# Kernel optimization log

Hardware: AMD Instinct MI355X
Metric: run time of the kernel (lower is better)

Reference implementation:

```python
import jax, jax.numpy as jnp
import numpy as np

D = 256
H = 8
HD = D // H
LN_EPS = 1e-5


def setup_inputs() -> dict:
    key = jax.random.key(0)
    ks = jax.random.split(key, 20)
    N = 768
    s = lambda *sh: 1.0 / np.sqrt(sh[-1])
    inp = {
        "features": jax.random.normal(ks[0], (N, D), jnp.float32),
        "boxes": jax.random.uniform(ks[1], (N, 4), jnp.float32),
        # MultiheadAttention params (torch layout: [out, in])
        "in_proj_w": jax.random.normal(ks[2], (3 * D, D), jnp.float32) * s(D),
        "in_proj_b": jnp.zeros((3 * D,), jnp.float32),
        "out_proj_w": jax.random.normal(ks[3], (D, D), jnp.float32) * s(D),
        "out_proj_b": jnp.zeros((D,), jnp.float32),
        # similarity_net params
        "w1": jax.random.normal(ks[4], (256, 3 * D + 3), jnp.float32) * s(3 * D + 3),
        "b1": jnp.zeros((256,), jnp.float32),
        "ln_g": jnp.ones((256,), jnp.float32),
        "ln_b": jnp.zeros((256,), jnp.float32),
        "w2": jax.random.normal(ks[5], (128, 256), jnp.float32) * s(256),
        "b2": jnp.zeros((128,), jnp.float32),
        "w3": jax.random.normal(ks[6], (64, 128), jnp.float32) * s(128),
        "b3": jnp.zeros((64,), jnp.float32),
        "w4": jax.random.normal(ks[7], (32, 64), jnp.float32) * s(64),
        "b4": jnp.zeros((32,), jnp.float32),
        "w5": jax.random.normal(ks[8], (1, 32), jnp.float32) * s(32),
        "b5": jnp.zeros((1,), jnp.float32),
    }
    return inp


def _mha(x, in_w, in_b, out_w, out_b):
    # x: [N, D]; torch nn.MultiheadAttention self-attention (eval mode)
    N = x.shape[0]
    qkv = x @ in_w.T + in_b                      # [N, 3D]
    q, k, v = jnp.split(qkv, 3, axis=-1)
    q = q.reshape(N, H, HD).transpose(1, 0, 2)   # [H, N, HD]
    k = k.reshape(N, H, HD).transpose(1, 0, 2)
    v = v.reshape(N, H, HD).transpose(1, 0, 2)
    scores = jnp.einsum("hnd,hmd->hnm", q, k) / np.sqrt(HD)
    attn = jax.nn.softmax(scores, axis=-1)
    o = jnp.einsum("hnm,hmd->hnd", attn, v)      # [H, N, HD]
    o = o.transpose(1, 0, 2).reshape(N, D)
    return o @ out_w.T + out_b


def reference(features, boxes, in_proj_w, in_proj_b, out_proj_w, out_proj_b,
              w1, b1, ln_g, ln_b, w2, b2, w3, b3, w4, b4, w5, b5):
    N = features.shape[0]
    att = _mha(features, in_proj_w, in_proj_b, out_proj_w, out_proj_b)  # [N, D]

    fi = jnp.broadcast_to(att[:, None, :], (N, N, D))
    fj = jnp.broadcast_to(att[None, :, :], (N, N, D))
    bi = boxes[:, None, :]
    bj = boxes[None, :, :]
    x_dist = jnp.abs(bi[:, :, 0] - bj[:, :, 0])
    y_diff = bi[:, :, 1] - bj[:, :, 1]
    spatial = jnp.stack([x_dist, jnp.abs(y_diff), y_diff], axis=-1)    # [N, N, 3]
    pairs = jnp.concatenate([fi, fj, fi * fj, spatial], axis=-1)       # [N, N, 3D+3]

    h = jax.nn.relu(pairs @ w1.T + b1)
    mu = jnp.mean(h, axis=-1, keepdims=True)
    var = jnp.var(h, axis=-1, keepdims=True)
    h = (h - mu) / jnp.sqrt(var + LN_EPS) * ln_g + ln_b
    h = jax.nn.relu(h @ w2.T + b2)
    h = jax.nn.relu(h @ w3.T + b3)
    h = jax.nn.relu(h @ w4.T + b4)
    logits = (h @ w5.T + b5)[..., 0]                                   # [N, N]

    eye = jnp.eye(N, dtype=logits.dtype)
    return logits * (1.0 - eye) - 1e9 * eye
```

## Files before the change

kernel.cpp:

```cpp
#include <hip/hip_runtime.h>


typedef __attribute__((ext_vector_type(8))) __bf16 bf16x8;
typedef __attribute__((ext_vector_type(4))) float f32x4;

__device__ __forceinline__ float bf2f(unsigned short u) {
    return __uint_as_float(((unsigned int)u) << 16);
}
__device__ __forceinline__ unsigned short f2bf(float f) {
    union { __bf16 b; unsigned short u; } cv;
    cv.b = (__bf16)f;
    return cv.u;
}
__device__ __forceinline__ int pk4_fp8(float a, float b, float c, float d) {
    int w = __builtin_amdgcn_cvt_pk_fp8_f32(a, b, 0, false);
    w = __builtin_amdgcn_cvt_pk_fp8_f32(c, d, w, true);
    return w;
}
__device__ __forceinline__ unsigned char f2fp8(float v) {
    return (unsigned char)(__builtin_amdgcn_cvt_pk_fp8_f32(v, 0.f, 0, false) & 0xff);
}

__global__ __launch_bounds__(256) void pack_all(
    const float* __restrict__ features, const float* __restrict__ in_proj_w,
    const float* __restrict__ out_proj_w, const float* __restrict__ w1,
    const float* __restrict__ w2, const float* __restrict__ w3,
    const float* __restrict__ w4, const float* __restrict__ b1,
    const float* __restrict__ ln_g, const float* __restrict__ ln_b,
    const float* __restrict__ b2, const float* __restrict__ out_proj_b,
    unsigned short* __restrict__ featb, unsigned short* __restrict__ inWb,
    unsigned short* __restrict__ WcatB, unsigned short* __restrict__ outWTb,
    unsigned short* __restrict__ wABb,
    unsigned char* __restrict__ w1c_f8, unsigned char* __restrict__ w2g_f8,
    unsigned char* __restrict__ w3_f8, unsigned char* __restrict__ w4_f8,
    float* __restrict__ bias768, float* __restrict__ c1, float* __restrict__ c2,
    float* __restrict__ biasZ)
{
    int t = blockIdx.x * 256 + threadIdx.x;
    if (t < 196608) {
        featb[t] = f2bf(features[t]);
    } else if (t < 393216) {
        int u = t - 196608; inWb[u] = f2bf(in_proj_w[u]);
    } else if (t < 458752) {
        int u = t - 393216; WcatB[u] = f2bf(out_proj_w[u]);
    } else if (t < 524288) {
        int u = t - 458752; int e = u >> 8, d = u & 255;
        outWTb[u] = f2bf(out_proj_w[d * 256 + e]);
    } else if (t < 655360) {
        int u = t - 524288; int n = u >> 8, k = u & 255;
        float v = (n < 256) ? w1[n * 771 + k] : w1[(n - 256) * 771 + 256 + k];
        wABb[u] = f2bf(v);
    } else if (t < 729088) {
        int u = t - 655360;
        int e = u & 7, lane = (u >> 3) & 63, f = u >> 9;
        int l15 = lane & 15, quad = lane >> 4;
        int mt = f & 15, kc = f >> 4;
        int o = mt * 16 + l15, k = kc * 32 + quad * 8 + e;
        float v;
        if (k < 256)            v = w1[o * 771 + 512 + k];
        else if (k < 259)       v = w1[o * 771 + 768 + (k - 256)];
        else                    v = 0.f;
        w1c_f8[u] = f2fp8(v);
    } else if (t < 761856) {
        int u = t - 729088;
        int e = u & 7, lane = (u >> 3) & 63, f = u >> 9;
        int l15 = lane & 15, quad = lane >> 4;
        int mt = f & 7, kc = f >> 3;
        int o = mt * 16 + l15, k = kc * 32 + quad * 8 + e;
        w2g_f8[u] = f2fp8(w2[o * 256 + k] * ln_g[k]);
    } else if (t < 770048) {
        int u = t - 761856;
        int e = u & 7, lane = (u >> 3) & 63, f = u >> 9;
        int l15 = lane & 15, quad = lane >> 4;
        int mt = f & 3, kc = f >> 2;
        int o = mt * 16 + l15, k = kc * 32 + quad * 8 + e;
        w3_f8[u] = f2fp8(w3[o * 128 + k]);
    } else if (t < 772096) {
        int u = t - 770048;
        int e = u & 7, lane = (u >> 3) & 63, f = u >> 9;
        int l15 = lane & 15, quad = lane >> 4;
        int mt = f & 1, kc = f >> 1;
        int o = mt * 16 + l15, k = kc * 32 + quad * 8 + e;
        w4_f8[u] = f2fp8(w4[o * 64 + k]);
    } else if (t < 772864) {
        int n = t - 772096;
        if (n < 256) bias768[n] = out_proj_b[n];
        else {
            int m = n - 256;
            float s = 0.f;
            for (int d = 0; d < 256; d += 4) {
                float4 ob = *reinterpret_cast<const float4*>(&out_proj_b[d]);
                const float* wr = (m < 256) ? &w1[m * 771 + d]
                                            : &w1[(m - 256) * 771 + 256 + d];
                float4 w = *reinterpret_cast<const float4*>(wr);
                s += ob.x * w.x + ob.y * w.y + ob.z * w.z + ob.w * w.w;
            }
            bias768[n] = s + ((m < 256) ? b1[m] : 0.f);
        }
    } else if (t < 772992) {
        int p = t - 772864;
        float s2 = 0.f, s1 = 0.f;
        for (int k = 0; k < 256; k += 4) {
            float4 w = *reinterpret_cast<const float4*>(&w2[p * 256 + k]);
            float4 g = *reinterpret_cast<const float4*>(&ln_g[k]);
            float4 lb = *reinterpret_cast<const float4*>(&ln_b[k]);
            s2 += g.x * w.x + g.y * w.y + g.z * w.z + g.w * w.w;
            s1 += lb.x * w.x + lb.y * w.y + lb.z * w.z + lb.w * w.w;
        }
        c2[p] = s2;
        c1[p] = s1 + b2[p];
    } else if (t < 773248) {
        biasZ[t - 772992] = 0.f;
    }
}

__global__ __launch_bounds__(256) void gemm_bf(
    const unsigned short* __restrict__ A, const unsigned short* __restrict__ W,
    const float* __restrict__ bias, float* __restrict__ Cf,
    unsigned short* __restrict__ Cbf, unsigned short* __restrict__ Vt,
    int N, int K, int ldc, int tcol0)
{
    const int wv = threadIdx.x >> 6, lane = threadIdx.x & 63;
    const int l15 = lane & 15, quad = lane >> 4;
    const int row0 = blockIdx.x * 64 + wv * 16;
    const int col0 = blockIdx.y * 64;
    f32x4 acc[4] = {};
    for (int kc = 0; kc < (K >> 5); ++kc) {
        bf16x8 a = *reinterpret_cast<const bf16x8*>(&A[(row0 + l15) * K + kc * 32 + quad * 8]);
#pragma unroll
        for (int ct = 0; ct < 4; ++ct) {
            bf16x8 b = *reinterpret_cast<const bf16x8*>(&W[(col0 + ct * 16 + l15) * K + kc * 32 + quad * 8]);
            acc[ct] = __builtin_amdgcn_mfma_f32_16x16x32_bf16(a, b, acc[ct], 0, 0, 0);
        }
    }
#pragma unroll
    for (int ct = 0; ct < 4; ++ct)
#pragma unroll
        for (int r = 0; r < 4; ++r) {
            int row = row0 + quad * 4 + r, col = col0 + ct * 16 + l15;
            float v = acc[ct][r] + bias[col];
            if (Vt && col >= tcol0) {
                Vt[(col - tcol0) * 768 + row] = f2bf(v);
            } else {
                if (Cf)  Cf[row * ldc + col] = v;
                if (Cbf) Cbf[row * ldc + col] = f2bf(v);
            }
        }
}

__global__ __launch_bounds__(256) void gemm_attab(
    const unsigned short* __restrict__ A, const unsigned short* __restrict__ W,
    const float* __restrict__ bias, float* __restrict__ att,
    unsigned short* __restrict__ attb, float* __restrict__ AB)
{
    const int wv = threadIdx.x >> 6, lane = threadIdx.x & 63;
    const int l15 = lane & 15, quad = lane >> 4;
    const int row0 = blockIdx.x * 64 + wv * 16;
    const int col0 = blockIdx.y * 64;
    f32x4 acc[4] = {};
    for (int kc = 0; kc < 8; ++kc) {
        bf16x8 a = *reinterpret_cast<const bf16x8*>(&A[(row0 + l15) * 256 + kc * 32 + quad * 8]);
#pragma unroll
        for (int ct = 0; ct < 4; ++ct) {
            bf16x8 b = *reinterpret_cast<const bf16x8*>(&W[(col0 + ct * 16 + l15) * 256 + kc * 32 + quad * 8]);
            acc[ct] = __builtin_amdgcn_mfma_f32_16x16x32_bf16(a, b, acc[ct], 0, 0, 0);
        }
    }
#pragma unroll
    for (int ct = 0; ct < 4; ++ct)
#pragma unroll
        for (int r = 0; r < 4; ++r) {
            int row = row0 + quad * 4 + r, col = col0 + ct * 16 + l15;
            float v = acc[ct][r] + bias[col];
            if (col < 256) {
                att[row * 256 + col] = v;
                attb[row * 256 + col] = f2bf(v);
            } else {
                AB[row * 512 + (col - 256)] = v;
            }
        }
}

#define SP 776

__global__ __launch_bounds__(256) void attn_mfma(
    const unsigned short* __restrict__ qkvb, const unsigned short* __restrict__ Vt,
    unsigned short* __restrict__ Obf)
{
    __shared__ __align__(16) unsigned short smS[64 * SP];
    const int h = blockIdx.x, q0 = blockIdx.y * 64, hb = h * 32;
    const int tid = threadIdx.x, wave = tid >> 6, lane = tid & 63;
    const int l15 = lane & 15, quad = lane >> 4;

    bf16x8 af[4];
#pragma unroll
    for (int mt = 0; mt < 4; ++mt)
        af[mt] = *reinterpret_cast<const bf16x8*>(&qkvb[(q0 + mt * 16 + l15) * 768 + hb + quad * 8]);
#pragma unroll
    for (int ct = 0; ct < 12; ++ct) {
        int n0 = wave * 192 + ct * 16;
        bf16x8 b = *reinterpret_cast<const bf16x8*>(&qkvb[(n0 + l15) * 768 + 256 + hb + quad * 8]);
#pragma unroll
        for (int mt = 0; mt < 4; ++mt) {
            f32x4 c = {};
            c = __builtin_amdgcn_mfma_f32_16x16x32_bf16(af[mt], b, c, 0, 0, 0);
#pragma unroll
            for (int r = 0; r < 4; ++r)
                smS[(mt * 16 + quad * 4 + r) * SP + n0 + l15] =
                    f2bf(c[r] * 0.17677669529663689f);
        }
    }
    __syncthreads();

    {
        const int row = tid >> 2, part = tid & 3;
        unsigned short* rp = &smS[row * SP + part * 192];
        float mx = -3.0e38f;
#pragma unroll
        for (int c8 = 0; c8 < 24; ++c8) {
            uint4 v = *reinterpret_cast<const uint4*>(&rp[c8 * 8]);
            const unsigned short* pe = reinterpret_cast<const unsigned short*>(&v);
#pragma unroll
            for (int e = 0; e < 8; ++e) mx = fmaxf(mx, bf2f(pe[e]));
        }
        mx = fmaxf(mx, __shfl_xor(mx, 1, 64));
        mx = fmaxf(mx, __shfl_xor(mx, 2, 64));
        float ls = 0.f;
#pragma unroll
        for (int c8 = 0; c8 < 24; ++c8) {
            uint4 v = *reinterpret_cast<const uint4*>(&rp[c8 * 8]);
            const unsigned short* pe = reinterpret_cast<const unsigned short*>(&v);
            unsigned short o8[8];
#pragma unroll
            for (int e = 0; e < 8; ++e) {
                float ev = __expf(bf2f(pe[e]) - mx);
                ls += ev;
                o8[e] = f2bf(ev);
            }
            *reinterpret_cast<uint4*>(&rp[c8 * 8]) = *reinterpret_cast<const uint4*>(o8);
        }
        ls += __shfl_xor(ls, 1, 64);
        ls += __shfl_xor(ls, 2, 64);
        float inv = 1.0f / ls;
#pragma unroll
        for (int c8 = 0; c8 < 24; ++c8) {
            uint4 v = *reinterpret_cast<const uint4*>(&rp[c8 * 8]);
            const unsigned short* pe = reinterpret_cast<const unsigned short*>(&v);
            unsigned short o8[8];
#pragma unroll
            for (int e = 0; e < 8; ++e) o8[e] = f2bf(bf2f(pe[e]) * inv);
            *reinterpret_cast<uint4*>(&rp[c8 * 8]) = *reinterpret_cast<const uint4*>(o8);
        }
    }
    f32x4 accp[2] = {};
    for (int kc = 0; kc < 24; ++kc) {
        bf16x8 a = *reinterpret_cast<const bf16x8*>(&smS[(wave * 16 + l15) * SP + kc * 32 + quad * 8]);
#pragma unroll
        for (int ct = 0; ct < 2; ++ct) {
            bf16x8 b = *reinterpret_cast<const bf16x8*>(&Vt[(hb + ct * 16 + l15) * 768 + kc * 32 + quad * 8]);
            accp[ct] = __builtin_amdgcn_mfma_f32_16x16x32_bf16(a, b, accp[ct], 0, 0, 0);
        }
    }
#pragma unroll
    for (int ct = 0; ct < 2; ++ct)
#pragma unroll
        for (int r = 0; r < 4; ++r) {
            int row = q0 + wave * 16 + quad * 4 + r;
            Obf[row * 256 + hb + ct * 16 + l15] = f2bf(accp[ct][r]);
        }
}

#define S1 296
#define S2 136
#define S3 72

__global__ __launch_bounds__(256, 4) void pair_mlp(
    const float* __restrict__ att, const unsigned short* __restrict__ attb,
    const float* __restrict__ AB,
    const unsigned char* __restrict__ w1c_f8, const unsigned char* __restrict__ w2g_f8,
    const unsigned char* __restrict__ w3_f8, const unsigned char* __restrict__ w4_f8,
    const float* __restrict__ boxes,
    const float* __restrict__ c1, const float* __restrict__ c2,
    const float* __restrict__ b3, const float* __restrict__ b4,
    const float* __restrict__ w5, const float* __restrict__ b5,
    float* __restrict__ out)
{
    __shared__ __align__(16) unsigned char smH[64 * S1];
    __shared__ float s_psum[64][4], s_pssq[64][4];
    __shared__ float s_mu[64], s_rs[64];
    __shared__ float s_l5[64][2];

    const int i    = blockIdx.x;
    const int j0   = blockIdx.y * 64;
    const int tid  = threadIdx.x;
    const int wave = tid >> 6;
    const int lane = tid & 63;
    const int l15  = lane & 15;
    const int quad = lane >> 4;

    {
        const int g = tid & 63;
        float4 fi4 = *reinterpret_cast<const float4*>(&att[i * 256 + g * 4]);
#pragma unroll
        for (int it = 0; it < 16; ++it) {
            int r = (tid >> 6) + it * 4;
            uint2 aj = *reinterpret_cast<const uint2*>(&attb[(j0 + r) * 256 + g * 4]);
            float a0 = __uint_as_float(aj.x << 16);
            float a1 = __uint_as_float(aj.x & 0xffff0000u);
            float a2 = __uint_as_float(aj.y << 16);
            float a3 = __uint_as_float(aj.y & 0xffff0000u);
            *reinterpret_cast<int*>(&smH[r * S1 + g * 4]) =
                pk4_fp8(a0 * fi4.x, a1 * fi4.y, a2 * fi4.z, a3 * fi4.w);
        }
    }
    if (tid < 64) {
        int j = j0 + tid;
        float xd = fabsf(boxes[i * 4 + 0] - boxes[j * 4 + 0]);
        float yd = boxes[i * 4 + 1] - boxes[j * 4 + 1];
        *reinterpret_cast<int*>(&smH[tid * S1 + 256]) = pk4_fp8(xd, fabsf(yd), yd, 0.f);
        *reinterpret_cast<int*>(&smH[tid * S1 + 260]) = 0;
        *reinterpret_cast<long long*>(&smH[tid * S1 + 264]) = 0;
        *reinterpret_cast<long long*>(&smH[tid * S1 + 272]) = 0;
        *reinterpret_cast<long long*>(&smH[tid * S1 + 280]) = 0;
    }
    __syncthreads();

    f32x4 acc1[4][4] = {};
    for (int kc = 0; kc < 9; ++kc) {
        long long a[4];
#pragma unroll
        for (int mt = 0; mt < 4; ++mt)
            a[mt] = *reinterpret_cast<const long long*>(&w1c_f8[((kc * 16 + wave * 4 + mt) * 64 + lane) * 8]);
#pragma unroll
        for (int nt = 0; nt < 4; ++nt) {
            long long b = *reinterpret_cast<const long long*>(&smH[(nt * 16 + l15) * S1 + kc * 32 + quad * 8]);
#pragma unroll
            for (int mt = 0; mt < 4; ++mt)
                acc1[mt][nt] = __builtin_amdgcn_mfma_f32_16x16x32_fp8_fp8(a[mt], b, acc1[mt][nt], 0, 0, 0);
        }
    }

    const int o0 = wave * 64;
    float vsum[4] = {}, vssq[4] = {};
#pragma unroll
    for (int mt = 0; mt < 4; ++mt) {
        int o = o0 + mt * 16 + quad * 4;
        float4 Ai = *reinterpret_cast<const float4*>(&AB[i * 512 + o]);
        float AiA[4] = {Ai.x, Ai.y, Ai.z, Ai.w};
#pragma unroll
        for (int nt = 0; nt < 4; ++nt) {
            int j = nt * 16 + l15;
            float4 Bj = *reinterpret_cast<const float4*>(&AB[(j0 + j) * 512 + 256 + o]);
            float BjA[4] = {Bj.x, Bj.y, Bj.z, Bj.w};
#pragma unroll
            for (int r = 0; r < 4; ++r) {
                float v = fmaxf(acc1[mt][nt][r] + AiA[r] + BjA[r], 0.f);
                acc1[mt][nt][r] = v;
                vsum[nt] += v; vssq[nt] += v * v;
            }
        }
    }
#pragma unroll
    for (int nt = 0; nt < 4; ++nt) {
        vsum[nt] += __shfl_xor(vsum[nt], 16, 64);
        vsum[nt] += __shfl_xor(vsum[nt], 32, 64);
        vssq[nt] += __shfl_xor(vssq[nt], 16, 64);
        vssq[nt] += __shfl_xor(vssq[nt], 32, 64);
    }
    if (quad == 0)
#pragma unroll
        for (int nt = 0; nt < 4; ++nt) {
            s_psum[nt * 16 + l15][wave] = vsum[nt];
            s_pssq[nt * 16 + l15][wave] = vssq[nt];
        }
    __syncthreads();
#pragma unroll
    for (int mt = 0; mt < 4; ++mt) {
        int o = o0 + mt * 16 + quad * 4;
#pragma unroll
        for (int nt = 0; nt < 4; ++nt) {
            int j = nt * 16 + l15;
            *reinterpret_cast<int*>(&smH[j * S1 + o]) =
                pk4_fp8(acc1[mt][nt][0], acc1[mt][nt][1], acc1[mt][nt][2], acc1[mt][nt][3]);
        }
    }
    if (wave == 0) {
        int j = lane;
        float sm = (s_psum[j][0] + s_psum[j][1] + s_psum[j][2] + s_psum[j][3]) * (1.0f / 256.0f);
        float sq = (s_pssq[j][0] + s_pssq[j][1] + s_pssq[j][2] + s_pssq[j][3]) * (1.0f / 256.0f);
        s_mu[j] = sm;
        s_rs[j] = rsqrtf(sq - sm * sm + 1e-5f);
    }
    __syncthreads();

    f32x4 acc2[2][4] = {};
    for (int kc = 0; kc < 8; ++kc) {
        long long a[2];
#pragma unroll
        for (int mt = 0; mt < 2; ++mt)
            a[mt] = *reinterpret_cast<const long long*>(&w2g_f8[((kc * 8 + wave * 2 + mt) * 64 + lane) * 8]);
#pragma unroll
        for (int nt = 0; nt < 4; ++nt) {
            long long b = *reinterpret_cast<const long long*>(&smH[(nt * 16 + l15) * S1 + kc * 32 + quad * 8]);
#pragma unroll
            for (int mt = 0; mt < 2; ++mt)
                acc2[mt][nt] = __builtin_amdgcn_mfma_f32_16x16x32_fp8_fp8(a[mt], b, acc2[mt][nt], 0, 0, 0);
        }
    }
    __syncthreads();
#pragma unroll
    for (int mt = 0; mt < 2; ++mt) {
        int p = wave * 32 + mt * 16 + quad * 4;
        float4 C1 = *reinterpret_cast<const float4*>(&c1[p]);
        float4 C2 = *reinterpret_cast<const float4*>(&c2[p]);
        float C1A[4] = {C1.x, C1.y, C1.z, C1.w};
        float C2A[4] = {C2.x, C2.y, C2.z, C2.w};
#pragma unroll
        for (int nt = 0; nt < 4; ++nt) {
            int j = nt * 16 + l15;
            float mu = s_mu[j], rs = s_rs[j];
            float vv[4];
#pragma unroll
            for (int r = 0; r < 4; ++r)
                vv[r] = fmaxf(rs * (acc2[mt][nt][r] - mu * C2A[r]) + C1A[r], 0.f);
            *reinterpret_cast<int*>(&smH[j * S2 + p]) = pk4_fp8(vv[0], vv[1], vv[2], vv[3]);
        }
    }
    __syncthreads();

    f32x4 acc3[4] = {};
    for (int kc = 0; kc < 4; ++kc) {
        long long a = *reinterpret_cast<const long long*>(&w3_f8[((kc * 4 + wave) * 64 + lane) * 8]);
#pragma unroll
        for (int nt = 0; nt < 4; ++nt) {
            long long b = *reinterpret_cast<const long long*>(&smH[(nt * 16 + l15) * S2 + kc * 32 + quad * 8]);
            acc3[nt] = __builtin_amdgcn_mfma_f32_16x16x32_fp8_fp8(a, b, acc3[nt], 0, 0, 0);
        }
    }
    __syncthreads();
    {
        int q = wave * 16 + quad * 4;
        float4 B3 = *reinterpret_cast<const float4*>(&b3[q]);
        float B3A[4] = {B3.x, B3.y, B3.z, B3.w};
#pragma unroll
        for (int nt = 0; nt < 4; ++nt) {
            int j = nt * 16 + l15;
            float vv[4];
#pragma unroll
            for (int r = 0; r < 4; ++r)
                vv[r] = fmaxf(acc3[nt][r] + B3A[r], 0.f);
            *reinterpret_cast<int*>(&smH[j * S3 + q]) = pk4_fp8(vv[0], vv[1], vv[2], vv[3]);
        }
    }
    __syncthreads();

    const int mt4 = wave & 1;
    const int jh  = wave >> 1;
    f32x4 acc4[2] = {};
#pragma unroll
    for (int kc = 0; kc < 2; ++kc) {
        long long a = *reinterpret_cast<const long long*>(&w4_f8[((kc * 2 + mt4) * 64 + lane) * 8]);
#pragma unroll
        for (int nt = 0; nt < 2; ++nt) {
            int j = jh * 32 + nt * 16 + l15;
            long long b = *reinterpret_cast<const long long*>(&smH[j * S3 + kc * 32 + quad * 8]);
            acc4[nt] = __builtin_amdgcn_mfma_f32_16x16x32_fp8_fp8(a, b, acc4[nt], 0, 0, 0);
        }
    }
    {
        int o4 = mt4 * 16 + quad * 4;
        float4 B4 = *reinterpret_cast<const float4*>(&b4[o4]);
        float4 W5 = *reinterpret_cast<const float4*>(&w5[o4]);
        float B4A[4] = {B4.x, B4.y, B4.z, B4.w};
        float W5A[4] = {W5.x, W5.y, W5.z, W5.w};
#pragma unroll
        for (int nt = 0; nt < 2; ++nt) {
            float part = 0.f;
#pragma unroll
            for (int r = 0; r < 4; ++r)
                part += fmaxf(acc4[nt][r] + B4A[r], 0.f) * W5A[r];
            part += __shfl_xor(part, 16, 64);
            part += __shfl_xor(part, 32, 64);
            if (quad == 0)
                s_l5[jh * 32 + nt * 16 + l15][mt4] = part;
        }
    }
    __syncthreads();
    if (tid < 64) {
        int j = j0 + tid;
        float v = s_l5[tid][0] + s_l5[tid][1] + b5[0];
        out[i * 768 + j] = (j == i) ? -1.0e9f : v;
    }
}

extern "C" void kernel_launch(void* const* d_in, const int* in_sizes, int n_in,
                              void* d_out, int out_size, void* d_ws, size_t ws_size,
                              hipStream_t stream)
{
    const float* features   = (const float*)d_in[0];
    const float* boxes      = (const float*)d_in[1];
    const float* in_proj_w  = (const float*)d_in[2];
    const float* in_proj_b  = (const float*)d_in[3];
    const float* out_proj_w = (const float*)d_in[4];
    const float* out_proj_b = (const float*)d_in[5];
    const float* w1  = (const float*)d_in[6];
    const float* b1  = (const float*)d_in[7];
    const float* ln_g = (const float*)d_in[8];
    const float* ln_b = (const float*)d_in[9];
    const float* w2  = (const float*)d_in[10];
    const float* b2  = (const float*)d_in[11];
    const float* w3  = (const float*)d_in[12];
    const float* b3  = (const float*)d_in[13];
    const float* w4  = (const float*)d_in[14];
    const float* b4  = (const float*)d_in[15];
    const float* w5  = (const float*)d_in[16];
    const float* b5  = (const float*)d_in[17];
    float* out = (float*)d_out;

    char* p = (char*)d_ws;
    unsigned short* qkvb  = (unsigned short*)p; p += 768 * 768 * 2;
    unsigned short* Vt    = (unsigned short*)p; p += 256 * 768 * 2;
    unsigned short* Obf   = (unsigned short*)p; p += 768 * 256 * 2;
    unsigned short* attb  = (unsigned short*)p; p += 768 * 256 * 2;
    float* att = (float*)p; p += 768 * 256 * 4;
    float* AB  = (float*)p; p += 768 * 512 * 4;
    unsigned short* featb  = (unsigned short*)p; p += 196608 * 2;
    unsigned short* inWb   = (unsigned short*)p; p += 196608 * 2;
    unsigned short* WcatB  = (unsigned short*)p; p += 196608 * 2;
    unsigned short* outWTb = (unsigned short*)p; p += 65536 * 2;
    unsigned short* wABb   = (unsigned short*)p; p += 131072 * 2;
    unsigned char* w1c_f8  = (unsigned char*)p; p += 73728;
    unsigned char* w2g_f8  = (unsigned char*)p; p += 32768;
    unsigned char* w3_f8   = (unsigned char*)p; p += 8192;
    unsigned char* w4_f8   = (unsigned char*)p; p += 2048;
    float* bias768 = (float*)p; p += 768 * 4;
    float* c1v     = (float*)p; p += 128 * 4;
    float* c2v     = (float*)p; p += 128 * 4;
    float* biasZ   = (float*)p; p += 256 * 4;

    pack_all<<<dim3(3021), dim3(256), 0, stream>>>(features, in_proj_w,
        out_proj_w, w1, w2, w3, w4, b1, ln_g, ln_b, b2, out_proj_b,
        featb, inWb, WcatB, outWTb, wABb, w1c_f8, w2g_f8, w3_f8, w4_f8,
        bias768, c1v, c2v, biasZ);
    gemm_bf<<<dim3(8, 4), dim3(256), 0, stream>>>(wABb, outWTb, biasZ,
        (float*)nullptr, WcatB + 65536, (unsigned short*)nullptr, 256, 256, 256, 1 << 30);
    gemm_bf<<<dim3(12, 12), dim3(256), 0, stream>>>(featb, inWb, in_proj_b,
        (float*)nullptr, qkvb, Vt, 768, 256, 768, 512);
    attn_mfma<<<dim3(8, 12), dim3(256), 0, stream>>>(qkvb, Vt, Obf);
    gemm_attab<<<dim3(12, 12), dim3(256), 0, stream>>>(Obf, WcatB, bias768,
        att, attb, AB);
    pair_mlp<<<dim3(768, 12), dim3(256), 0, stream>>>(att, attb, AB,
        w1c_f8, w2g_f8, w3_f8, w4_f8, boxes, c1v, c2v,
        b3, b4, w5, b5, out);
}
```

Before: 304.7 us.

## Fold QKV and weight-product GEMMs into packing kernel, split attention finer

The separate bf16 conversion pass and two gemm_bf launches are removed. The pack kernel now does the QKV projection straight from fp32 inputs, converting on load, and computes the W1·out_proj product as a scalar dot-product block. This cuts two launches and the intermediate bf16 buffers. Attention now uses 32-query tiles for twice as many blocks. pair_mlp drops the bf16 att copy and uses separate shared buffers per layer, which removes two barriers at the cost of more LDS per block and possibly lower occupancy.

```diff
diff --git a/kernel.cpp b/kernel.cpp
--- a/kernel.cpp
+++ b/kernel.cpp
@@ -12,6 +12,9 @@
     cv.b = (__bf16)f;
     return cv.u;
 }
+__device__ __forceinline__ unsigned pk2(float lo, float hi) {
+    return (unsigned)f2bf(lo) | ((unsigned)f2bf(hi) << 16);
+}
 __device__ __forceinline__ int pk4_fp8(float a, float b, float c, float d) {
     int w = __builtin_amdgcn_cvt_pk_fp8_f32(a, b, 0, false);
     w = __builtin_amdgcn_cvt_pk_fp8_f32(c, d, w, true);
@@ -20,138 +23,138 @@
 __device__ __forceinline__ unsigned char f2fp8(float v) {
     return (unsigned char)(__builtin_amdgcn_cvt_pk_fp8_f32(v, 0.f, 0, false) & 0xff);
 }
+__device__ __forceinline__ bf16x8 load8f_bf(const float* p) {
+    float4 a = *reinterpret_cast<const float4*>(p);
+    float4 b = *reinterpret_cast<const float4*>(p + 4);
+    union { bf16x8 v; unsigned u[4]; } cv;
+    cv.u[0] = pk2(a.x, a.y); cv.u[1] = pk2(a.z, a.w);
+    cv.u[2] = pk2(b.x, b.y); cv.u[3] = pk2(b.z, b.w);
+    return cv.v;
+}
 
 __global__ __launch_bounds__(256) void pack_all(
     const float* __restrict__ features, const float* __restrict__ in_proj_w,
-    const float* __restrict__ out_proj_w, const float* __restrict__ w1,
-    const float* __restrict__ w2, const float* __restrict__ w3,
-    const float* __restrict__ w4, const float* __restrict__ b1,
-    const float* __restrict__ ln_g, const float* __restrict__ ln_b,
-    const float* __restrict__ b2, const float* __restrict__ out_proj_b,
-    unsigned short* __restrict__ featb, unsigned short* __restrict__ inWb,
-    unsigned short* __restrict__ WcatB, unsigned short* __restrict__ outWTb,
-    unsigned short* __restrict__ wABb,
+    const float* __restrict__ in_proj_b, const float* __restrict__ out_proj_w,
+    const float* __restrict__ w1, const float* __restrict__ w2,
+    const float* __restrict__ w3, const float* __restrict__ w4,
+    const float* __restrict__ b1, const float* __restrict__ ln_g,
+    const float* __restrict__ ln_b, const float* __restrict__ b2,
+    const float* __restrict__ out_proj_b,
+    unsigned short* __restrict__ qkvb, unsigned short* __restrict__ Vt,
+    unsigned short* __restrict__ WcatB,
     unsigned char* __restrict__ w1c_f8, unsigned char* __restrict__ w2g_f8,
     unsigned char* __restrict__ w3_f8, unsigned char* __restrict__ w4_f8,
-    float* __restrict__ bias768, float* __restrict__ c1, float* __restrict__ c2,
-    float* __restrict__ biasZ)
+    float* __restrict__ bias768, float* __restrict__ c1, float* __restrict__ c2)
 {
-    int t = blockIdx.x * 256 + threadIdx.x;
-    if (t < 196608) {
-        featb[t] = f2bf(features[t]);
-    } else if (t < 393216) {
-        int u = t - 196608; inWb[u] = f2bf(in_proj_w[u]);
-    } else if (t < 458752) {
-        int u = t - 393216; WcatB[u] = f2bf(out_proj_w[u]);
-    } else if (t < 524288) {
-        int u = t - 458752; int e = u >> 8, d = u & 255;
-        outWTb[u] = f2bf(out_proj_w[d * 256 + e]);
-    } else if (t < 655360) {
-        int u = t - 524288; int n = u >> 8, k = u & 255;
-        float v = (n < 256) ? w1[n * 771 + k] : w1[(n - 256) * 771 + 256 + k];
-        wABb[u] = f2bf(v);
-    } else if (t < 729088) {
-        int u = t - 655360;
-        int e = u & 7, lane = (u >> 3) & 63, f = u >> 9;
-        int l15 = lane & 15, quad = lane >> 4;
-        int mt = f & 15, kc = f >> 4;
-        int o = mt * 16 + l15, k = kc * 32 + quad * 8 + e;
-        float v;
-        if (k < 256)            v = w1[o * 771 + 512 + k];
-        else if (k < 259)       v = w1[o * 771 + 768 + (k - 256)];
-        else                    v = 0.f;
-        w1c_f8[u] = f2fp8(v);
-    } else if (t < 761856) {
-        int u = t - 729088;
-        int e = u & 7, lane = (u >> 3) & 63, f = u >> 9;
-        int l15 = lane & 15, quad = lane >> 4;
-        int mt = f & 7, kc = f >> 3;
-        int o = mt * 16 + l15, k = kc * 32 + quad * 8 + e;
-        w2g_f8[u] = f2fp8(w2[o * 256 + k] * ln_g[k]);
-    } else if (t < 770048) {
-        int u = t - 761856;
-        int e = u & 7, lane = (u >> 3) & 63, f = u >> 9;
-        int l15 = lane & 15, quad = lane >> 4;
-        int mt = f & 3, kc = f >> 2;
-        int o = mt * 16 + l15, k = kc * 32 + quad * 8 + e;
-        w3_f8[u] = f2fp8(w3[o * 128 + k]);
-    } else if (t < 772096) {
-        int u = t - 770048;
-        int e = u & 7, lane = (u >> 3) & 63, f = u >> 9;
-        int l15 = lane & 15, quad = lane >> 4;
-        int mt = f & 1, kc = f >> 1;
-        int o = mt * 16 + l15, k = kc * 32 + quad * 8 + e;
-        w4_f8[u] = f2fp8(w4[o * 64 + k]);
-    } else if (t < 772864) {
-        int n = t - 772096;
-        if (n < 256) bias768[n] = out_proj_b[n];
-        else {
-            int m = n - 256;
-            float s = 0.f;
-            for (int d = 0; d < 256; d += 4) {
-                float4 ob = *reinterpret_cast<const float4*>(&out_proj_b[d]);
-                const float* wr = (m < 256) ? &w1[m * 771 + d]
-                                            : &w1[(m - 256) * 771 + 256 + d];
-                float4 w = *reinterpret_cast<const float4*>(wr);
-                s += ob.x * w.x + ob.y * w.y + ob.z * w.z + ob.w * w.w;
+    const int blk = blockIdx.x;
+    if (blk < 716) {
+        int t = blk * 256 + threadIdx.x;
+        if (t < 65536) {
+            WcatB[t] = f2bf(out_proj_w[t]);
+        } else if (t < 139264) {
+            int u = t - 65536;
+            int e = u & 7, lane = (u >> 3) & 63, f = u >> 9;
+            int l15 = lane & 15, quad = lane >> 4;
+            int ct = f & 15, kc = f >> 4;
+            int o = ct * 16 + l15, k = kc * 32 + quad * 8 + e;
+            float v;
+            if (k < 256)       v = w1[o * 771 + 512 + k];
+            else if (k < 259)  v = w1[o * 771 + 768 + (k - 256)];
+            else               v = 0.f;
+            w1c_f8[u] = f2fp8(v);
+        } else if (t < 172032) {
+            int u = t - 139264;
+            int e = u & 7, lane = (u >> 3) & 63, f = u >> 9;
+            int l15 = lane & 15, quad = lane >> 4;
+            int ct = f & 7, kc = f >> 3;
+            int o = ct * 16 + l15, k = kc * 32 + quad * 8 + e;
+            w2g_f8[u] = f2fp8(w2[o * 256 + k] * ln_g[k]);
+        } else if (t < 180224) {
+            int u = t - 172032;
+            int e = u & 7, lane = (u >> 3) & 63, f = u >> 9;
+            int l15 = lane & 15, quad = lane >> 4;
+            int ct = f & 3, kc = f >> 2;
+            int o = ct * 16 + l15, k = kc * 32 + quad * 8 + e;
+            w3_f8[u] = f2fp8(w3[o * 128 + k]);
+        } else if (t < 182272) {
+            int u = t - 180224;
+            int e = u & 7, lane = (u >> 3) & 63, f = u >> 9;
+            int l15 = lane & 15, quad = lane >> 4;
+            int ct = f & 1, kc = f >> 1;
+            int o = ct * 16 + l15, k = kc * 32 + quad * 8 + e;
+            w4_f8[u] = f2fp8(w4[o * 64 + k]);
+        } else if (t < 183040) {
+            int n = t - 182272;
+            if (n < 256) bias768[n] = out_proj_b[n];
+            else {
+                int m = n - 256;
+                float s = 0.f;
+                for (int d = 0; d < 256; d += 4) {
+                    float4 ob = *reinterpret_cast<const float4*>(&out_proj_b[d]);
+                    const float* wr = (m < 256) ? &w1[m * 771 + d]
+                                                : &w1[(m - 256) * 771 + 256 + d];
+                    float4 w = *reinterpret_cast<const float4*>(wr);
+                    s += ob.x * w.x + ob.y * w.y + ob.z * w.z + ob.w * w.w;
+                }
+                bias768[n] = s + ((m < 256) ? b1[m] : 0.f);
             }
-            bias768[n] = s + ((m < 256) ? b1[m] : 0.f);
-        }
-    } else if (t < 772992) {
-        int p = t - 772864;
-        float s2 = 0.f, s1 = 0.f;
-        for (int k = 0; k < 256; k += 4) {
-            float4 w = *reinterpret_cast<const float4*>(&w2[p * 256 + k]);
-            float4 g = *reinterpret_cast<const float4*>(&ln_g[k]);
-            float4 lb = *reinterpret_cast<const float4*>(&ln_b[k]);
-            s2 += g.x * w.x + g.y * w.y + g.z * w.z + g.w * w.w;
-            s1 += lb.x * w.x + lb.y * w.y + lb.z * w.z + lb.w * w.w;
-        }
-        c2[p] = s2;
-        c1[p] = s1 + b2[p];
-    } else if (t < 773248) {
-        biasZ[t - 772992] = 0.f;
-    }
-}
-
-__global__ __launch_bounds__(256) void gemm_bf(
-    const unsigned short* __restrict__ A, const unsigned short* __restrict__ W,
-    const float* __restrict__ bias, float* __restrict__ Cf,
-    unsigned short* __restrict__ Cbf, unsigned short* __restrict__ Vt,
-    int N, int K, int ldc, int tcol0)
-{
-    const int wv = threadIdx.x >> 6, lane = threadIdx.x & 63;
-    const int l15 = lane & 15, quad = lane >> 4;
-    const int row0 = blockIdx.x * 64 + wv * 16;
-    const int col0 = blockIdx.y * 64;
-    f32x4 acc[4] = {};
-    for (int kc = 0; kc < (K >> 5); ++kc) {
-        bf16x8 a = *reinterpret_cast<const bf16x8*>(&A[(row0 + l15) * K + kc * 32 + quad * 8]);
-#pragma unroll
-        for (int ct = 0; ct < 4; ++ct) {
-            bf16x8 b = *reinterpret_cast<const bf16x8*>(&W[(col0 + ct * 16 + l15) * K + kc * 32 + quad * 8]);
-            acc[ct] = __builtin_amdgcn_mfma_f32_16x16x32_bf16(a, b, acc[ct], 0, 0, 0);
-        }
-    }
-#pragma unroll
-    for (int ct = 0; ct < 4; ++ct)
-#pragma unroll
-        for (int r = 0; r < 4; ++r) {
-            int row = row0 + quad * 4 + r, col = col0 + ct * 16 + l15;
-            float v = acc[ct][r] + bias[col];
-            if (Vt && col >= tcol0) {
-                Vt[(col - tcol0) * 768 + row] = f2bf(v);
-            } else {
-                if (Cf)  Cf[row * ldc + col] = v;
-                if (Cbf) Cbf[row * ldc + col] = f2bf(v);
+        } else if (t < 183168) {
+            int p = t - 183040;
+            float s2 = 0.f, s1 = 0.f;
+            for (int k = 0; k < 256; k += 4) {
+                float4 w = *reinterpret_cast<const float4*>(&w2[p * 256 + k]);
+                float4 g = *reinterpret_cast<const float4*>(&ln_g[k]);
+                float4 lb = *reinterpret_cast<const float4*>(&ln_b[k]);
+                s2 += g.x * w.x + g.y * w.y + g.z * w.z + g.w * w.w;
+                s1 += lb.x * w.x + lb.y * w.y + lb.z * w.z + lb.w * w.w;
             }
-        }
+            c2[p] = s2;
+            c1[p] = s1 + b2[p];
+        }
+    } else if (blk < 1228) {
+        const int n = blk - 716, e = threadIdx.x;
+        const float* wrow = (n < 256) ? &w1[n * 771] : &w1[(n - 256) * 771 + 256];
+        float acc = 0.f;
+        for (int d = 0; d < 256; d += 4) {
+            float4 w = *reinterpret_cast<const float4*>(&wrow[d]);
+            acc += w.x * out_proj_w[(d + 0) * 256 + e];
+            acc += w.y * out_proj_w[(d + 1) * 256 + e];
+            acc += w.z * out_proj_w[(d + 2) * 256 + e];
+            acc += w.w * out_proj_w[(d + 3) * 256 + e];
+        }
+        WcatB[(256 + n) * 256 + e] = f2bf(acc);
+    } else {
+        const int q = blk - 1228;
+        const int bm = q % 12, bn = q / 12;
+        const int wv = threadIdx.x >> 6, lane = threadIdx.x & 63;
+        const int l15 = lane & 15, quad = lane >> 4;
+        const int row0 = bm * 64 + wv * 16;
+        const int col0 = bn * 64;
+        f32x4 acc[4] = {};
+        for (int kc = 0; kc < 8; ++kc) {
+            bf16x8 a = load8f_bf(&features[(row0 + l15) * 256 + kc * 32 + quad * 8]);
+#pragma unroll
+            for (int ct = 0; ct < 4; ++ct) {
+                bf16x8 b = load8f_bf(&in_proj_w[(col0 + ct * 16 + l15) * 256 + kc * 32 + quad * 8]);
+                acc[ct] = __builtin_amdgcn_mfma_f32_16x16x32_bf16(a, b, acc[ct], 0, 0, 0);
+            }
+        }
+#pragma unroll
+        for (int ct = 0; ct < 4; ++ct)
+#pragma unroll
+            for (int r = 0; r < 4; ++r) {
+                int row = row0 + quad * 4 + r, col = col0 + ct * 16 + l15;
+                float v = acc[ct][r] + in_proj_b[col];
+                if (col < 512) qkvb[row * 768 + col] = f2bf(v);
+                else           Vt[(col - 512) * 768 + row] = f2bf(v);
+            }
+    }
 }
 
 __global__ __launch_bounds__(256) void gemm_attab(
     const unsigned short* __restrict__ A, const unsigned short* __restrict__ W,
     const float* __restrict__ bias, float* __restrict__ att,
-    unsigned short* __restrict__ attb, float* __restrict__ AB)
+    float* __restrict__ AB)
 {
     const int wv = threadIdx.x >> 6, lane = threadIdx.x & 63;
     const int l15 = lane & 15, quad = lane >> 4;
@@ -172,12 +175,8 @@
         for (int r = 0; r < 4; ++r) {
             int row = row0 + quad * 4 + r, col = col0 + ct * 16 + l15;
             float v = acc[ct][r] + bias[col];
-            if (col < 256) {
-                att[row * 256 + col] = v;
-                attb[row * 256 + col] = f2bf(v);
-            } else {
-                AB[row * 512 + (col - 256)] = v;
-            }
+            if (col < 256) att[row * 256 + col] = v;
+            else           AB[row * 512 + (col - 256)] = v;
         }
 }
 
@@ -187,21 +186,21 @@
     const unsigned short* __restrict__ qkvb, const unsigned short* __restrict__ Vt,
     unsigned short* __restrict__ Obf)
 {
-    __shared__ __align__(16) unsigned short smS[64 * SP];
-    const int h = blockIdx.x, q0 = blockIdx.y * 64, hb = h * 32;
+    __shared__ __align__(16) unsigned short smS[32 * SP];
+    const int h = blockIdx.x, q0 = blockIdx.y * 32, hb = h * 32;
     const int tid = threadIdx.x, wave = tid >> 6, lane = tid & 63;
     const int l15 = lane & 15, quad = lane >> 4;
 
-    bf16x8 af[4];
-#pragma unroll
-    for (int mt = 0; mt < 4; ++mt)
+    bf16x8 af[2];
+#pragma unroll
+    for (int mt = 0; mt < 2; ++mt)
         af[mt] = *reinterpret_cast<const bf16x8*>(&qkvb[(q0 + mt * 16 + l15) * 768 + hb + quad * 8]);
 #pragma unroll
     for (int ct = 0; ct < 12; ++ct) {
         int n0 = wave * 192 + ct * 16;
         bf16x8 b = *reinterpret_cast<const bf16x8*>(&qkvb[(n0 + l15) * 768 + 256 + hb + quad * 8]);
 #pragma unroll
-        for (int mt = 0; mt < 4; ++mt) {
+        for (int mt = 0; mt < 2; ++mt) {
             f32x4 c = {};
             c = __builtin_amdgcn_mfma_f32_16x16x32_bf16(af[mt], b, c, 0, 0, 0);
 #pragma unroll
@@ -213,11 +212,11 @@
     __syncthreads();
 
     {
-        const int row = tid >> 2, part = tid & 3;
-        unsigned short* rp = &smS[row * SP + part * 192];
+        const int row = tid >> 3, part = tid & 7;
+        unsigned short* rp = &smS[row * SP + part * 96];
         float mx = -3.0e38f;
 #pragma unroll
-        for (int c8 = 0; c8 < 24; ++c8) {
+        for (int c8 = 0; c8 < 12; ++c8) {
             uint4 v = *reinterpret_cast<const uint4*>(&rp[c8 * 8]);
             const unsigned short* pe = reinterpret_cast<const unsigned short*>(&v);
 #pragma unroll
@@ -225,9 +224,10 @@
         }
         mx = fmaxf(mx, __shfl_xor(mx, 1, 64));
         mx = fmaxf(mx, __shfl_xor(mx, 2, 64));
+        mx = fmaxf(mx, __shfl_xor(mx, 4, 64));
         float ls = 0.f;
 #pragma unroll
-        for (int c8 = 0; c8 < 24; ++c8) {
+        for (int c8 = 0; c8 < 12; ++c8) {
             uint4 v = *reinterpret_cast<const uint4*>(&rp[c8 * 8]);
             const unsigned short* pe = reinterpret_cast<const unsigned short*>(&v);
             unsigned short o8[8];
@@ -241,9 +241,10 @@
         }
         ls += __shfl_xor(ls, 1, 64);
         ls += __shfl_xor(ls, 2, 64);
+        ls += __shfl_xor(ls, 4, 64);
         float inv = 1.0f / ls;
 #pragma unroll
-        for (int c8 = 0; c8 < 24; ++c8) {
+        for (int c8 = 0; c8 < 12; ++c8) {
             uint4 v = *reinterpret_cast<const uint4*>(&rp[c8 * 8]);
             const unsigned short* pe = reinterpret_cast<const unsigned short*>(&v);
             unsigned short o8[8];
@@ -252,22 +253,20 @@
             *reinterpret_cast<uint4*>(&rp[c8 * 8]) = *reinterpret_cast<const uint4*>(o8);
         }
     }
-    f32x4 accp[2] = {};
+    __syncthreads();
+
+    const int row0 = (wave >> 1) * 16, cg = wave & 1;
+    f32x4 accp = {};
     for (int kc = 0; kc < 24; ++kc) {
-        bf16x8 a = *reinterpret_cast<const bf16x8*>(&smS[(wave * 16 + l15) * SP + kc * 32 + quad * 8]);
-#pragma unroll
-        for (int ct = 0; ct < 2; ++ct) {
-            bf16x8 b = *reinterpret_cast<const bf16x8*>(&Vt[(hb + ct * 16 + l15) * 768 + kc * 32 + quad * 8]);
-            accp[ct] = __builtin_amdgcn_mfma_f32_16x16x32_bf16(a, b, accp[ct], 0, 0, 0);
-        }
-    }
-#pragma unroll
-    for (int ct = 0; ct < 2; ++ct)
-#pragma unroll
-        for (int r = 0; r < 4; ++r) {
-            int row = q0 + wave * 16 + quad * 4 + r;
-            Obf[row * 256 + hb + ct * 16 + l15] = f2bf(accp[ct][r]);
-        }
+        bf16x8 a = *reinterpret_cast<const bf16x8*>(&smS[(row0 + l15) * SP + kc * 32 + quad * 8]);
+        bf16x8 b = *reinterpret_cast<const bf16x8*>(&Vt[(hb + cg * 16 + l15) * 768 + kc * 32 + quad * 8]);
+        accp = __builtin_amdgcn_mfma_f32_16x16x32_bf16(a, b, accp, 0, 0, 0);
+    }
+#pragma unroll
+    for (int r = 0; r < 4; ++r) {
+        int row = q0 + row0 + quad * 4 + r;
+        Obf[row * 256 + hb + cg * 16 + l15] = f2bf(accp[r]);
+    }
 }
 
 #define S1 296
@@ -275,8 +274,7 @@
 #define S3 72
 
 __global__ __launch_bounds__(256, 4) void pair_mlp(
-    const float* __restrict__ att, const unsigned short* __restrict__ attb,
-    const float* __restrict__ AB,
+    const float* __restrict__ att, const float* __restrict__ AB,
     const unsigned char* __restrict__ w1c_f8, const unsigned char* __restrict__ w2g_f8,
     const unsigned char* __restrict__ w3_f8, const unsigned char* __restrict__ w4_f8,
     const float* __restrict__ boxes,
@@ -286,6 +284,8 @@
     float* __restrict__ out)
 {
     __shared__ __align__(16) unsigned char smH[64 * S1];
+    __shared__ __align__(16) unsigned char smH2[64 * S2];
+    __shared__ __align__(16) unsigned char smH3[64 * S3];
     __shared__ float s_psum[64][4], s_pssq[64][4];
     __shared__ float s_mu[64], s_rs[64];
     __shared__ float s_l5[64][2];
@@ -304,13 +304,9 @@
 #pragma unroll
         for (int it = 0; it < 16; ++it) {
             int r = (tid >> 6) + it * 4;
-            uint2 aj = *reinterpret_cast<const uint2*>(&attb[(j0 + r) * 256 + g * 4]);
-            float a0 = __uint_as_float(aj.x << 16);
-            float a1 = __uint_as_float(aj.x & 0xffff0000u);
-            float a2 = __uint_as_float(aj.y << 16);
-            float a3 = __uint_as_float(aj.y & 0xffff0000u);
+            float4 aj = *reinterpret_cast<const float4*>(&att[(j0 + r) * 256 + g * 4]);
             *reinterpret_cast<int*>(&smH[r * S1 + g * 4]) =
-                pk4_fp8(a0 * fi4.x, a1 * fi4.y, a2 * fi4.z, a3 * fi4.w);
+                pk4_fp8(aj.x * fi4.x, aj.y * fi4.y, aj.z * fi4.z, aj.w * fi4.w);
         }
     }
     if (tid < 64) {
@@ -407,7 +403,6 @@
                 acc2[mt][nt] = __builtin_amdgcn_mfma_f32_16x16x32_fp8_fp8(a[mt], b, acc2[mt][nt], 0, 0, 0);
         }
     }
-    __syncthreads();
 #pragma unroll
     for (int mt = 0; mt < 2; ++mt) {
         int p = wave * 32 + mt * 16 + quad * 4;
@@ -423,7 +418,7 @@
 #pragma unroll
             for (int r = 0; r < 4; ++r)
                 vv[r] = fmaxf(rs * (acc2[mt][nt][r] - mu * C2A[r]) + C1A[r], 0.f);
-            *reinterpret_cast<int*>(&smH[j * S2 + p]) = pk4_fp8(vv[0], vv[1], vv[2], vv[3]);
+            *reinterpret_cast<int*>(&smH2[j * S2 + p]) = pk4_fp8(vv[0], vv[1], vv[2], vv[3]);
         }
     }
     __syncthreads();
@@ -433,11 +428,10 @@
         long long a = *reinterpret_cast<const long long*>(&w3_f8[((kc * 4 + wave) * 64 + lane) * 8]);
 #pragma unroll
         for (int nt = 0; nt < 4; ++nt) {
-            long long b = *reinterpret_cast<const long long*>(&smH[(nt * 16 + l15) * S2 + kc * 32 + quad * 8]);
+            long long b = *reinterpret_cast<const long long*>(&smH2[(nt * 16 + l15) * S2 + kc * 32 + quad * 8]);
             acc3[nt] = __builtin_amdgcn_mfma_f32_16x16x32_fp8_fp8(a, b, acc3[nt], 0, 0, 0);
         }
     }
-    __syncthreads();
     {
         int q = wave * 16 + quad * 4;
         float4 B3 = *reinterpret_cast<const float4*>(&b3[q]);
@@ -449,7 +443,7 @@
 #pragma unroll
             for (int r = 0; r < 4; ++r)
                 vv[r] = fmaxf(acc3[nt][r] + B3A[r], 0.f);
-            *reinterpret_cast<int*>(&smH[j * S3 + q]) = pk4_fp8(vv[0], vv[1], vv[2], vv[3]);
+            *reinterpret_cast<int*>(&smH3[j * S3 + q]) = pk4_fp8(vv[0], vv[1], vv[2], vv[3]);
         }
     }
     __syncthreads();
@@ -463,7 +457,7 @@
 #pragma unroll
         for (int nt = 0; nt < 2; ++nt) {
             int j = jh * 32 + nt * 16 + l15;
-            long long b = *reinterpret_cast<const long long*>(&smH[j * S3 + kc * 32 + quad * 8]);
+            long long b = *reinterpret_cast<const long long*>(&smH3[j * S3 + kc * 32 + quad * 8]);
             acc4[nt] = __builtin_amdgcn_mfma_f32_16x16x32_fp8_fp8(a, b, acc4[nt], 0, 0, 0);
         }
     }
@@ -521,14 +515,9 @@
     unsigned short* qkvb  = (unsigned short*)p; p += 768 * 768 * 2;
     unsigned short* Vt    = (unsigned short*)p; p += 256 * 768 * 2;
     unsigned short* Obf   = (unsigned short*)p; p += 768 * 256 * 2;
-    unsigned short* attb  = (unsigned short*)p; p += 768 * 256 * 2;
+    unsigned short* WcatB = (unsigned short*)p; p += 196608 * 2;
     float* att = (float*)p; p += 768 * 256 * 4;
     float* AB  = (float*)p; p += 768 * 512 * 4;
-    unsigned short* featb  = (unsigned short*)p; p += 196608 * 2;
-    unsigned short* inWb   = (unsigned short*)p; p += 196608 * 2;
-    unsigned short* WcatB  = (unsigned short*)p; p += 196608 * 2;
-    unsigned short* outWTb = (unsigned short*)p; p += 65536 * 2;
-    unsigned short* wABb   = (unsigned short*)p; p += 131072 * 2;
     unsigned char* w1c_f8  = (unsigned char*)p; p += 73728;
     unsigned char* w2g_f8  = (unsigned char*)p; p += 32768;
     unsigned char* w3_f8   = (unsigned char*)p; p += 8192;
@@ -536,20 +525,14 @@
     float* bias768 = (float*)p; p += 768 * 4;
     float* c1v     = (float*)p; p += 128 * 4;
     float* c2v     = (float*)p; p += 128 * 4;
-    float* biasZ   = (float*)p; p += 256 * 4;
-
-    pack_all<<<dim3(3021), dim3(256), 0, stream>>>(features, in_proj_w,
-        out_proj_w, w1, w2, w3, w4, b1, ln_g, ln_b, b2, out_proj_b,
-        featb, inWb, WcatB, outWTb, wABb, w1c_f8, w2g_f8, w3_f8, w4_f8,
-        bias768, c1v, c2v, biasZ);
-    gemm_bf<<<dim3(8, 4), dim3(256), 0, stream>>>(wABb, outWTb, biasZ,
-        (float*)nullptr, WcatB + 65536, (unsigned short*)nullptr, 256, 256, 256, 1 << 30);
-    gemm_bf<<<dim3(12, 12), dim3(256), 0, stream>>>(featb, inWb, in_proj_b,
-        (float*)nullptr, qkvb, Vt, 768, 256, 768, 512);
-    attn_mfma<<<dim3(8, 12), dim3(256), 0, stream>>>(qkvb, Vt, Obf);
+
+    pack_all<<<dim3(1372), dim3(256), 0, stream>>>(features, in_proj_w,
+        in_proj_b, out_proj_w, w1, w2, w3, w4, b1, ln_g, ln_b, b2, out_proj_b,
+        qkvb, Vt, WcatB, w1c_f8, w2g_f8, w3_f8, w4_f8, bias768, c1v, c2v);
+    attn_mfma<<<dim3(8, 24), dim3(256), 0, stream>>>(qkvb, Vt, Obf);
     gemm_attab<<<dim3(12, 12), dim3(256), 0, stream>>>(Obf, WcatB, bias768,
-        att, attb, AB);
-    pair_mlp<<<dim3(768, 12), dim3(256), 0, stream>>>(att, attb, AB,
+        att, AB);
+    pair_mlp<<<dim3(768, 12), dim3(256), 0, stream>>>(att, AB,
         w1c_f8, w2g_f8, w3_f8, w4_f8, boxes, c1v, c2v,
         b3, b4, w5, b5, out);
 }
```

Measured after the change: 301.2 us. No clear change (-1.2%).
